# Optimization experiments

Measured on AMD Instinct MI355X. Metric: run time of the kernel, lower is better.

## Reference

```python
import jax, jax.numpy as jnp
import numpy as np


def _knn_ood(embeddings, bank, k, out_h, out_w):
    # embeddings: [B, D, h, w] ; bank: [N, D]
    B, D, h, w = embeddings.shape
    q = embeddings.transpose(0, 2, 3, 1).reshape(B * h * w, D)  # [Q, D] queries (per-pixel)
    # squared euclidean via ||q||^2 + ||b||^2 - 2 q.b (single GEMM, no python loop over batch)
    q2 = jnp.sum(q * q, axis=1, keepdims=True)                  # [Q, 1]
    b2 = jnp.sum(bank * bank, axis=1)[None, :]                  # [1, N]
    d2 = q2 + b2 - 2.0 * (q @ bank.T)                           # [Q, N]
    d = jnp.sqrt(jnp.maximum(d2, 1e-12))                        # euclidean, like sklearn
    neg_topk, _ = jax.lax.top_k(-d, k)                          # k smallest distances
    scores = jnp.mean(-neg_topk, axis=1).reshape(B, 1, h, w)    # mean distance to k-NN
    # F.interpolate(..., mode='bilinear', align_corners=False) == half-pixel bilinear resize
    return jax.image.resize(scores, (B, 1, out_h, out_w), method="bilinear")


def setup_inputs() -> dict:
    key = jax.random.key(0)
    k1, k2 = jax.random.split(key)
    B, D, h, w = 4, 128, 32, 32
    N = 50000
    return {
        "embeddings": jax.random.normal(k1, (B, D, h, w), dtype=jnp.float32),
        "bank": jax.random.normal(k2, (N, D), dtype=jnp.float32),
        "k": 5,
        "out_h": 512,
        "out_w": 512,
    }


def reference(embeddings, bank, k, out_h, out_w):
    return _knn_ood(embeddings, bank, k, out_h, out_w)
```

## Files before the change

### kernel.cpp

```cpp
#include <hip/hip_runtime.h>

typedef unsigned short u16;
typedef __attribute__((ext_vector_type(4))) unsigned short u16x4;
typedef __attribute__((ext_vector_type(8))) unsigned short u16x8;
typedef __attribute__((ext_vector_type(8))) __bf16 bf16x8;
typedef __attribute__((ext_vector_type(4))) float f32x4;

#define N_BANK  50000
#define NPAD    50048
#define NCHUNKS 782
#define SEGS    32
#define NCPAD   800
#define DIM     128
#define NQ      4096
#define CHUNK_B 16384

#define WS_BANKBF 0u
#define WS_B2     12812288u
#define WS_QBF    13012480u
#define WS_Q2     14061056u
#define WS_SCORES 14077440u
#define WS_MINBUF 14093824u
#define WS_NEED_PAIRS 27201024u

__device__ __forceinline__ u16 f2bf(float f) {
  unsigned int x = __float_as_uint(f);
  x += 0x7fffu + ((x >> 16) & 1u);
  return (u16)(x >> 16);
}
__device__ __forceinline__ u16 f2bf_up(float f) {
  unsigned int b = __float_as_uint(f);
  u16 h = (u16)(b >> 16);
  if (!(b >> 31) && (b & 0xffffu)) h++;
  return h;
}
__device__ __forceinline__ float bf2f(u16 h) {
  return __uint_as_float(((unsigned int)h) << 16);
}

#define SINS5(T0, T1, T2, T3, T4, x)                                  \
  {                                                                   \
    bool c3 = (x) < T3, c2 = (x) < T2, c1 = (x) < T1, c0 = (x) < T0;  \
    float nx_ = fminf((x), T4);                                       \
    T4 = c3 ? T3 : nx_;                                               \
    T3 = c3 ? (c2 ? T2 : (x)) : T3;                                   \
    T2 = c2 ? (c1 ? T1 : (x)) : T2;                                   \
    T1 = c1 ? (c0 ? T0 : (x)) : T1;                                   \
    T0 = c0 ? (x) : T0;                                               \
  }

__device__ __forceinline__ void gload_lds16(const void* g, void* l) {
  __builtin_amdgcn_global_load_lds(
      (const __attribute__((address_space(1))) void*)g,
      (__attribute__((address_space(3))) void*)l, 16, 0, 0);
}

__global__ __launch_bounds__(256) void prep_bank(const float* __restrict__ bank,
                                                 u16* __restrict__ bb,
                                                 float* __restrict__ b2) {
  int row = blockIdx.x * 8 + (threadIdx.x >> 5);
  int cc  = threadIdx.x & 31;
  bool valid = row < N_BANK;
  f32x4 v = f32x4{0.f, 0.f, 0.f, 0.f};
  if (valid) v = *reinterpret_cast<const f32x4*>(bank + (size_t)row * DIM + cc * 4);
  float s = v.x * v.x + v.y * v.y + v.z * v.z + v.w * v.w;
#pragma unroll
  for (int o = 16; o > 0; o >>= 1) s += __shfl_xor(s, o, 32);
  u16x4 u;
  u.x = f2bf(v.x); u.y = f2bf(v.y); u.z = f2bf(v.z); u.w = f2bf(v.w);
  *reinterpret_cast<u16x4*>(bb + (size_t)row * DIM + cc * 4) = u;
  if (cc == 0) b2[row] = valid ? s : 1e30f;
}

__global__ __launch_bounds__(256) void prep_q(const float* __restrict__ emb,
                                              u16* __restrict__ qb,
                                              float* __restrict__ q2) {
  int q = blockIdx.x * 256 + threadIdx.x;
  int b = q >> 10, yx = q & 1023;
  const float* src = emb + (size_t)b * 131072 + yx;
  float s = 0.f;
#pragma unroll
  for (int d0 = 0; d0 < 16; ++d0) {
    u16x8 u;
#pragma unroll
    for (int j = 0; j < 8; ++j) {
      float v = src[(d0 * 8 + j) * 1024];
      s += v * v;
      u[j] = f2bf(v);
    }
    *reinterpret_cast<u16x8*>(qb + (size_t)q * DIM + d0 * 8) = u;
  }
  q2[q] = s;
}

template <bool PAIRS>
__global__ __launch_bounds__(512) void pass1_kernel(const u16* __restrict__ bankbf,
                                                    const float* __restrict__ b2,
                                                    const u16* __restrict__ qbf,
                                                    void* __restrict__ minbuf) {
  __shared__ char smc[2 * CHUNK_B];
  __shared__ unsigned int mintile[6400];
  const int tid = threadIdx.x;
  const int w = tid >> 6, l = tid & 63;
  const int l15 = l & 15, lhi = l >> 4;
  const int qgi = blockIdx.x & 15, seg = blockIdx.x >> 4;
  const int qbase = qgi * 256 + w * 32;

  for (int i = tid; i < 6400; i += 512) mintile[i] = 0x7F807F80u;

  bf16x8 bqA[4], bqB[4];
  {
    const u16* qa = qbf + (size_t)(qbase + l15) * DIM + lhi * 8;
#pragma unroll
    for (int kk = 0; kk < 4; ++kk) {
      bqA[kk] = *reinterpret_cast<const bf16x8*>(qa + kk * 32);
      bqB[kk] = *reinterpret_cast<const bf16x8*>(qa + 16 * DIM + kk * 32);
    }
  }

  auto stage = [&](int cc, int buf) {
    const char* gb = (const char*)bankbf + (size_t)cc * CHUNK_B;
#pragma unroll
    for (int i = 0; i < 2; ++i) {
      int x  = i * 8192 + tid * 16;
      int sx = x ^ (((x >> 8) & 7) << 4);
      gload_lds16(gb + sx, smc + buf * CHUNK_B + i * 8192 + w * 1024);
    }
  };

  stage(seg, 0);
  __syncthreads();
  int cur = 0;
  int s = 0;
  for (int c = seg; c < NCHUNKS; c += SEGS, ++s) {
    if (c + SEGS < NCHUNKS) stage(c + SEGS, cur ^ 1);
    const char* sb = smc + cur * CHUNK_B;
    float m1A = 3e38f, m2A = 3e38f, m1B = 3e38f, m2B = 3e38f;
#pragma unroll
    for (int t = 0; t < 4; ++t) {
      f32x4 b2v = *reinterpret_cast<const f32x4*>(b2 + c * 64 + t * 16 + lhi * 4);
      bf16x8 af[4];
#pragma unroll
      for (int kk = 0; kk < 4; ++kk) {
        int p  = (t * 16 + l15) * 256 + kk * 64 + lhi * 16;
        int ph = p ^ (((p >> 8) & 7) << 4);
        af[kk] = *reinterpret_cast<const bf16x8*>(sb + ph);
      }
      f32x4 accA = f32x4{0.f, 0.f, 0.f, 0.f};
      f32x4 accB = f32x4{0.f, 0.f, 0.f, 0.f};
#pragma unroll
      for (int kk = 0; kk < 4; ++kk) {
        accA = __builtin_amdgcn_mfma_f32_16x16x32_bf16(af[kk], bqA[kk], accA, 0, 0, 0);
        accB = __builtin_amdgcn_mfma_f32_16x16x32_bf16(af[kk], bqB[kk], accB, 0, 0, 0);
      }
#pragma unroll
      for (int j = 0; j < 4; ++j) {
        float sA = fmaf(-2.f, accA[j], b2v[j]);
        float sB = fmaf(-2.f, accB[j], b2v[j]);
        if (PAIRS) {
          float t1 = fminf(m1A, sA);
          m2A = fminf(m2A, fmaxf(m1A, sA));
          m1A = t1;
          float t2 = fminf(m1B, sB);
          m2B = fminf(m2B, fmaxf(m1B, sB));
          m1B = t2;
        } else {
          m1A = fminf(m1A, sA);
          m1B = fminf(m1B, sB);
        }
      }
    }
#pragma unroll
    for (int o = 16; o <= 32; o <<= 1) {
      float o1 = __shfl_xor(m1A, o);
      if (PAIRS) {
        float o2 = __shfl_xor(m2A, o);
        m2A = fminf(fminf(m2A, o2), fmaxf(m1A, o1));
      }
      m1A = fminf(m1A, o1);
      float p1 = __shfl_xor(m1B, o);
      if (PAIRS) {
        float p2 = __shfl_xor(m2B, o);
        m2B = fminf(fminf(m2B, p2), fmaxf(m1B, p1));
      }
      m1B = fminf(m1B, p1);
    }
    if (l < 16) {
      unsigned int pA, pB;
      if (PAIRS) {
        pA = ((unsigned int)f2bf(m2A) << 16) | (unsigned int)f2bf(m1A);
        pB = ((unsigned int)f2bf(m2B) << 16) | (unsigned int)f2bf(m1B);
      } else {
        pA = f2bf_up(m1A);
        pB = f2bf_up(m1B);
      }
      mintile[(w * 32 + l) * 25 + s] = pA;
      mintile[(w * 32 + 16 + l) * 25 + s] = pB;
    }
    __syncthreads();
    cur ^= 1;
  }

  if (PAIRS) {
    unsigned int* mb = (unsigned int*)minbuf;
    for (int i = tid; i < 6400; i += 512) {
      int qloc = i / 25, j = i - qloc * 25;
      mb[(size_t)(qgi * 256 + qloc) * NCPAD + seg * 25 + j] = mintile[i];
    }
  } else {
    u16* mb = (u16*)minbuf;
    for (int i = tid; i < 6400; i += 512) {
      int qloc = i / 25, j = i - qloc * 25;
      mb[(size_t)(qgi * 256 + qloc) * NCPAD + seg * 25 + j] = (u16)mintile[i];
    }
  }
}

template <bool PAIRS>
__global__ __launch_bounds__(256) void pass2_kernel(const u16* __restrict__ bankbf,
                                                    const float* __restrict__ b2,
                                                    const u16* __restrict__ qbf,
                                                    const float* __restrict__ q2,
                                                    const void* __restrict__ minbuf,
                                                    float* __restrict__ scores) {
  const int w = threadIdx.x >> 6, l = threadIdx.x & 63;
  const int q = blockIdx.x * 4 + w;

  unsigned int vals[13];
  if (PAIRS) {
    const unsigned int* row = (const unsigned int*)minbuf + (size_t)q * NCPAD;
#pragma unroll
    for (int r = 0; r < 13; ++r) {
      int col = r * 64 + l;
      vals[r] = (col < NCPAD) ? row[col] : 0x7F807F80u;
    }
  } else {
    const u16* row = (const u16*)minbuf + (size_t)q * NCPAD;
#pragma unroll
    for (int r = 0; r < 13; ++r) {
      int col = r * 64 + l;
      vals[r] = (col < NCPAD) ? (unsigned int)row[col] : 0x7F80u;
    }
  }

  float T0 = 3e38f, T1 = 3e38f, T2_ = 3e38f, T3 = 3e38f, T4 = 3e38f;
#pragma unroll
  for (int r = 0; r < 13; ++r) {
    float m1v = bf2f((u16)(vals[r] & 0xffffu));
    SINS5(T0, T1, T2_, T3, T4, m1v);
    if (PAIRS) {
      float m2v = bf2f((u16)(vals[r] >> 16));
      SINS5(T0, T1, T2_, T3, T4, m2v);
    }
  }
#pragma unroll
  for (int sft = 1; sft < 64; sft <<= 1) {
    float p0 = __shfl_xor(T0, sft), p1 = __shfl_xor(T1, sft), p2 = __shfl_xor(T2_, sft),
          p3 = __shfl_xor(T3, sft), p4 = __shfl_xor(T4, sft);
    SINS5(T0, T1, T2_, T3, T4, p0);
    SINS5(T0, T1, T2_, T3, T4, p1);
    SINS5(T0, T1, T2_, T3, T4, p2);
    SINS5(T0, T1, T2_, T3, T4, p3);
    SINS5(T0, T1, T2_, T3, T4, p4);
  }
  const float thr = PAIRS ? (T4 + fabsf(T4) * 0.01f + 2.5f)
                          : (T4 + fabsf(T4) * 0.01f + 0.02f);

  float F0 = 3e38f, F1 = 3e38f, F2_ = 3e38f, F3 = 3e38f, F4 = 3e38f;
  unsigned long long msk[13];
  unsigned long long anym = 0ull;
#pragma unroll
  for (int r = 0; r < 13; ++r) {
    float m1v = bf2f((u16)(vals[r] & 0xffffu));
    bool flag;
    if (PAIRS) {
      float m2v = bf2f((u16)(vals[r] >> 16));
      flag = (m2v <= thr);
      if (!flag) {
        SINS5(F0, F1, F2_, F3, F4, m1v);
        SINS5(F0, F1, F2_, F3, F4, m2v);
      }
    } else {
      flag = (m1v <= thr);
    }
    msk[r] = __ballot(flag);
    anym |= msk[r];
  }

  if (anym) {
    u16x8 qu[16];
#pragma unroll
    for (int g = 0; g < 16; ++g)
      qu[g] = *reinterpret_cast<const u16x8*>(qbf + (size_t)q * DIM + g * 8);
    for (int r = 0; r < 13; ++r) {
      unsigned long long mset = msk[r];
      while (mset) {
        int bit = __ffsll((long long)mset) - 1;
        mset &= mset - 1;
        int col = r * 64 + bit;
        int sgi = col / 25, sj = col - sgi * 25;
        int chunk = sgi + sj * SEGS;
        int rowid = chunk * 64 + l;
        const u16x8* bp = (const u16x8*)(bankbf + (size_t)rowid * DIM);
        float dot = 0.f;
#pragma unroll
        for (int g = 0; g < 16; ++g) {
          u16x8 bb = bp[g];
#pragma unroll
          for (int e = 0; e < 8; ++e)
            dot = fmaf(bf2f(bb[e]), bf2f(qu[g][e]), dot);
        }
        float d = fmaf(-2.f, dot, b2[rowid]);
        SINS5(F0, F1, F2_, F3, F4, d);
      }
    }
  }
#pragma unroll
  for (int sft = 1; sft < 64; sft <<= 1) {
    float p0 = __shfl_xor(F0, sft), p1 = __shfl_xor(F1, sft), p2 = __shfl_xor(F2_, sft),
          p3 = __shfl_xor(F3, sft), p4 = __shfl_xor(F4, sft);
    SINS5(F0, F1, F2_, F3, F4, p0);
    SINS5(F0, F1, F2_, F3, F4, p1);
    SINS5(F0, F1, F2_, F3, F4, p2);
    SINS5(F0, F1, F2_, F3, F4, p3);
    SINS5(F0, F1, F2_, F3, F4, p4);
  }
  if (l == 0) {
    float q2v = q2[q];
    float sc = sqrtf(fmaxf(q2v + F0, 1e-12f)) + sqrtf(fmaxf(q2v + F1, 1e-12f)) +
               sqrtf(fmaxf(q2v + F2_, 1e-12f)) + sqrtf(fmaxf(q2v + F3, 1e-12f)) +
               sqrtf(fmaxf(q2v + F4, 1e-12f));
    scores[q] = sc * 0.2f;
  }
}

__global__ __launch_bounds__(256) void resize_kernel(const float* __restrict__ scores,
                                                     float* __restrict__ out) {
  int idx = blockIdx.x * 256 + threadIdx.x;
  int b = idx >> 18;
  int rem = idx & 262143;
  int oy = rem >> 9, ox = rem & 511;
  float sx = (ox + 0.5f) * 0.0625f - 0.5f;
  float sy = (oy + 0.5f) * 0.0625f - 0.5f;
  float fx0 = floorf(sx), fy0 = floorf(sy);
  int x0 = (int)fx0, y0 = (int)fy0;
  float fx = sx - fx0, fy = sy - fy0;
  int x0c = x0 < 0 ? 0 : (x0 > 31 ? 31 : x0);
  int x1c = (x0 + 1) < 0 ? 0 : ((x0 + 1) > 31 ? 31 : (x0 + 1));
  int y0c = y0 < 0 ? 0 : (y0 > 31 ? 31 : y0);
  int y1c = (y0 + 1) < 0 ? 0 : ((y0 + 1) > 31 ? 31 : (y0 + 1));
  const float* sb = scores + (b << 10);
  float v00 = sb[y0c * 32 + x0c], v01 = sb[y0c * 32 + x1c];
  float v10 = sb[y1c * 32 + x0c], v11 = sb[y1c * 32 + x1c];
  float v0 = v00 + (v01 - v00) * fx;
  float v1 = v10 + (v11 - v10) * fx;
  out[idx] = v0 + (v1 - v0) * fy;
}

extern "C" void kernel_launch(void* const* d_in, const int* in_sizes, int n_in,
                              void* d_out, int out_size, void* d_ws, size_t ws_size,
                              hipStream_t stream) {
  const float* emb  = (const float*)d_in[0];
  const float* bank = (const float*)d_in[1];
  float* out = (float*)d_out;
  char* ws = (char*)d_ws;

  u16*   bankbf = (u16*)(ws + WS_BANKBF);
  float* b2     = (float*)(ws + WS_B2);
  u16*   qbf    = (u16*)(ws + WS_QBF);
  float* q2     = (float*)(ws + WS_Q2);
  float* scores = (float*)(ws + WS_SCORES);
  void*  minbuf = (void*)(ws + WS_MINBUF);

  prep_bank<<<NPAD / 8, 256, 0, stream>>>(bank, bankbf, b2);
  prep_q<<<NQ / 256, 256, 0, stream>>>(emb, qbf, q2);
  if (ws_size >= (size_t)WS_NEED_PAIRS) {
    pass1_kernel<true><<<16 * SEGS, 512, 0, stream>>>(bankbf, b2, qbf, minbuf);
    pass2_kernel<true><<<NQ / 4, 256, 0, stream>>>(bankbf, b2, qbf, q2, minbuf, scores);
  } else {
    pass1_kernel<false><<<16 * SEGS, 512, 0, stream>>>(bankbf, b2, qbf, minbuf);
    pass2_kernel<false><<<NQ / 4, 256, 0, stream>>>(bankbf, b2, qbf, q2, minbuf, scores);
  }
  resize_kernel<<<(NQ * 256) / 256, 256, 0, stream>>>(scores, out);
}
```

Before: 177.0 us.

## Fuse prep kernels, widen pass1 query tiles, fold -2 scaling, vectorize resize

```diff
diff --git a/kernel.cpp b/kernel.cpp
--- a/kernel.cpp
+++ b/kernel.cpp
@@ -14,6 +14,8 @@
 #define DIM     128
 #define NQ      4096
 #define CHUNK_B 16384
+#define NBANKBLK 6256
+#define NQBLK    64
 
 #define WS_BANKBF 0u
 #define WS_B2     12812288u
@@ -21,18 +23,11 @@
 #define WS_Q2     14061056u
 #define WS_SCORES 14077440u
 #define WS_MINBUF 14093824u
-#define WS_NEED_PAIRS 27201024u
 
 __device__ __forceinline__ u16 f2bf(float f) {
   unsigned int x = __float_as_uint(f);
   x += 0x7fffu + ((x >> 16) & 1u);
   return (u16)(x >> 16);
-}
-__device__ __forceinline__ u16 f2bf_up(float f) {
-  unsigned int b = __float_as_uint(f);
-  u16 h = (u16)(b >> 16);
-  if (!(b >> 31) && (b & 0xffffu)) h++;
-  return h;
 }
 __device__ __forceinline__ float bf2f(u16 h) {
   return __uint_as_float(((unsigned int)h) << 16);
@@ -55,203 +50,196 @@
       (__attribute__((address_space(3))) void*)l, 16, 0, 0);
 }
 
-__global__ __launch_bounds__(256) void prep_bank(const float* __restrict__ bank,
-                                                 u16* __restrict__ bb,
-                                                 float* __restrict__ b2) {
-  int row = blockIdx.x * 8 + (threadIdx.x >> 5);
-  int cc  = threadIdx.x & 31;
-  bool valid = row < N_BANK;
-  f32x4 v = f32x4{0.f, 0.f, 0.f, 0.f};
-  if (valid) v = *reinterpret_cast<const f32x4*>(bank + (size_t)row * DIM + cc * 4);
-  float s = v.x * v.x + v.y * v.y + v.z * v.z + v.w * v.w;
-#pragma unroll
-  for (int o = 16; o > 0; o >>= 1) s += __shfl_xor(s, o, 32);
-  u16x4 u;
-  u.x = f2bf(v.x); u.y = f2bf(v.y); u.z = f2bf(v.z); u.w = f2bf(v.w);
-  *reinterpret_cast<u16x4*>(bb + (size_t)row * DIM + cc * 4) = u;
-  if (cc == 0) b2[row] = valid ? s : 1e30f;
-}
-
-__global__ __launch_bounds__(256) void prep_q(const float* __restrict__ emb,
-                                              u16* __restrict__ qb,
-                                              float* __restrict__ q2) {
-  int q = blockIdx.x * 256 + threadIdx.x;
-  int b = q >> 10, yx = q & 1023;
-  const float* src = emb + (size_t)b * 131072 + yx;
-  float s = 0.f;
-#pragma unroll
-  for (int d0 = 0; d0 < 16; ++d0) {
-    u16x8 u;
-#pragma unroll
-    for (int j = 0; j < 8; ++j) {
-      float v = src[(d0 * 8 + j) * 1024];
-      s += v * v;
-      u[j] = f2bf(v);
-    }
-    *reinterpret_cast<u16x8*>(qb + (size_t)q * DIM + d0 * 8) = u;
-  }
-  q2[q] = s;
-}
-
-template <bool PAIRS>
-__global__ __launch_bounds__(512) void pass1_kernel(const u16* __restrict__ bankbf,
-                                                    const float* __restrict__ b2,
-                                                    const u16* __restrict__ qbf,
-                                                    void* __restrict__ minbuf) {
+__global__ __launch_bounds__(256) void prep_kernel(const float* __restrict__ emb,
+                                                   const float* __restrict__ bank,
+                                                   u16* __restrict__ bb,
+                                                   float* __restrict__ b2,
+                                                   u16* __restrict__ qb,
+                                                   float* __restrict__ q2) {
+  const int tid = threadIdx.x;
+  if (blockIdx.x < NBANKBLK) {
+    int row = blockIdx.x * 8 + (tid >> 5);
+    int cc  = tid & 31;
+    bool valid = row < N_BANK;
+    f32x4 v = f32x4{0.f, 0.f, 0.f, 0.f};
+    if (valid) v = *reinterpret_cast<const f32x4*>(bank + (size_t)row * DIM + cc * 4);
+    float s = v.x * v.x + v.y * v.y + v.z * v.z + v.w * v.w;
+#pragma unroll
+    for (int o = 16; o > 0; o >>= 1) s += __shfl_xor(s, o, 32);
+    u16x4 u;
+    u.x = f2bf(-2.f * v.x); u.y = f2bf(-2.f * v.y);
+    u.z = f2bf(-2.f * v.z); u.w = f2bf(-2.f * v.w);
+    *reinterpret_cast<u16x4*>(bb + (size_t)row * DIM + cc * 4) = u;
+    if (cc == 0) b2[row] = valid ? s : 1e30f;
+  } else {
+    __shared__ float part[256];
+    int qb0 = (blockIdx.x - NBANKBLK) * 64;
+    int ql = tid & 63, p = tid >> 6;
+    int q = qb0 + ql;
+    int b = q >> 10, yx = q & 1023;
+    const float* src = emb + (size_t)b * 131072 + (size_t)p * 32 * 1024 + yx;
+    float s = 0.f;
+#pragma unroll
+    for (int d8 = 0; d8 < 4; ++d8) {
+      u16x8 u;
+#pragma unroll
+      for (int j = 0; j < 8; ++j) {
+        float v = src[(d8 * 8 + j) * 1024];
+        s += v * v;
+        u[j] = f2bf(v);
+      }
+      *reinterpret_cast<u16x8*>(qb + (size_t)q * DIM + p * 32 + d8 * 8) = u;
+    }
+    part[tid] = s;
+    __syncthreads();
+    if (p == 0) q2[q] = part[ql] + part[64 + ql] + part[128 + ql] + part[192 + ql];
+  }
+}
+
+__global__ __launch_bounds__(256, 2) void pass1_kernel(const u16* __restrict__ bankbf,
+                                                       const float* __restrict__ b2,
+                                                       const u16* __restrict__ qbf,
+                                                       unsigned int* __restrict__ minbuf) {
   __shared__ char smc[2 * CHUNK_B];
   __shared__ unsigned int mintile[6400];
   const int tid = threadIdx.x;
   const int w = tid >> 6, l = tid & 63;
   const int l15 = l & 15, lhi = l >> 4;
   const int qgi = blockIdx.x & 15, seg = blockIdx.x >> 4;
-  const int qbase = qgi * 256 + w * 32;
-
-  for (int i = tid; i < 6400; i += 512) mintile[i] = 0x7F807F80u;
-
-  bf16x8 bqA[4], bqB[4];
-  {
-    const u16* qa = qbf + (size_t)(qbase + l15) * DIM + lhi * 8;
+  const int qbase = qgi * 256 + w * 64;
+
+  for (int i = tid; i < 6400; i += 256) mintile[i] = 0x7F807F80u;
+
+  bf16x8 bq[16];
+#pragma unroll
+  for (int sg = 0; sg < 4; ++sg)
+#pragma unroll
+    for (int kk = 0; kk < 4; ++kk)
+      bq[sg * 4 + kk] = *reinterpret_cast<const bf16x8*>(
+          qbf + (size_t)(qbase + sg * 16 + l15) * DIM + kk * 32 + lhi * 8);
+
+  int ph[16];
+#pragma unroll
+  for (int t = 0; t < 4; ++t)
 #pragma unroll
     for (int kk = 0; kk < 4; ++kk) {
-      bqA[kk] = *reinterpret_cast<const bf16x8*>(qa + kk * 32);
-      bqB[kk] = *reinterpret_cast<const bf16x8*>(qa + 16 * DIM + kk * 32);
-    }
-  }
+      int p = (t * 16 + l15) * 256 + kk * 64 + lhi * 16;
+      ph[t * 4 + kk] = p ^ (((p >> 8) & 7) << 4);
+    }
 
   auto stage = [&](int cc, int buf) {
     const char* gb = (const char*)bankbf + (size_t)cc * CHUNK_B;
 #pragma unroll
-    for (int i = 0; i < 2; ++i) {
-      int x  = i * 8192 + tid * 16;
+    for (int i = 0; i < 4; ++i) {
+      int x  = i * 4096 + tid * 16;
       int sx = x ^ (((x >> 8) & 7) << 4);
-      gload_lds16(gb + sx, smc + buf * CHUNK_B + i * 8192 + w * 1024);
+      gload_lds16(gb + sx, smc + buf * CHUNK_B + i * 4096 + w * 1024);
     }
   };
-
+  auto loadb2 = [&](int cc, f32x4* dst) {
+#pragma unroll
+    for (int t = 0; t < 4; ++t)
+      dst[t] = *reinterpret_cast<const f32x4*>(b2 + cc * 64 + t * 16 + lhi * 4);
+  };
+
+  auto process = [&](const char* sb, const f32x4* bv, int s) {
+    float m1[4], m2[4];
+#pragma unroll
+    for (int sg = 0; sg < 4; ++sg) { m1[sg] = 3e38f; m2[sg] = 3e38f; }
+#pragma unroll
+    for (int t = 0; t < 4; ++t) {
+      bf16x8 af[4];
+#pragma unroll
+      for (int kk = 0; kk < 4; ++kk)
+        af[kk] = *reinterpret_cast<const bf16x8*>(sb + ph[t * 4 + kk]);
+      f32x4 acc[4];
+#pragma unroll
+      for (int sg = 0; sg < 4; ++sg) acc[sg] = bv[t];
+#pragma unroll
+      for (int kk = 0; kk < 4; ++kk)
+#pragma unroll
+        for (int sg = 0; sg < 4; ++sg)
+          acc[sg] = __builtin_amdgcn_mfma_f32_16x16x32_bf16(af[kk], bq[sg * 4 + kk],
+                                                            acc[sg], 0, 0, 0);
+#pragma unroll
+      for (int sg = 0; sg < 4; ++sg)
+#pragma unroll
+        for (int j = 0; j < 4; ++j) {
+          float sv = acc[sg][j];
+          float t1 = fminf(m1[sg], sv);
+          m2[sg] = fminf(m2[sg], fmaxf(m1[sg], sv));
+          m1[sg] = t1;
+        }
+    }
+#pragma unroll
+    for (int sg = 0; sg < 4; ++sg) {
+#pragma unroll
+      for (int o = 16; o <= 32; o <<= 1) {
+        float o1 = __shfl_xor(m1[sg], o);
+        float o2 = __shfl_xor(m2[sg], o);
+        m2[sg] = fminf(fminf(m2[sg], o2), fmaxf(m1[sg], o1));
+        m1[sg] = fminf(m1[sg], o1);
+      }
+      if (l < 16)
+        mintile[(w * 64 + sg * 16 + l15) * 25 + s] =
+            ((unsigned int)f2bf(m2[sg]) << 16) | (unsigned int)f2bf(m1[sg]);
+    }
+  };
+
+  f32x4 b2A[4], b2B[4];
   stage(seg, 0);
+  loadb2(seg, b2A);
   __syncthreads();
-  int cur = 0;
-  int s = 0;
-  for (int c = seg; c < NCHUNKS; c += SEGS, ++s) {
-    if (c + SEGS < NCHUNKS) stage(c + SEGS, cur ^ 1);
-    const char* sb = smc + cur * CHUNK_B;
-    float m1A = 3e38f, m2A = 3e38f, m1B = 3e38f, m2B = 3e38f;
-#pragma unroll
-    for (int t = 0; t < 4; ++t) {
-      f32x4 b2v = *reinterpret_cast<const f32x4*>(b2 + c * 64 + t * 16 + lhi * 4);
-      bf16x8 af[4];
-#pragma unroll
-      for (int kk = 0; kk < 4; ++kk) {
-        int p  = (t * 16 + l15) * 256 + kk * 64 + lhi * 16;
-        int ph = p ^ (((p >> 8) & 7) << 4);
-        af[kk] = *reinterpret_cast<const bf16x8*>(sb + ph);
-      }
-      f32x4 accA = f32x4{0.f, 0.f, 0.f, 0.f};
-      f32x4 accB = f32x4{0.f, 0.f, 0.f, 0.f};
-#pragma unroll
-      for (int kk = 0; kk < 4; ++kk) {
-        accA = __builtin_amdgcn_mfma_f32_16x16x32_bf16(af[kk], bqA[kk], accA, 0, 0, 0);
-        accB = __builtin_amdgcn_mfma_f32_16x16x32_bf16(af[kk], bqB[kk], accB, 0, 0, 0);
-      }
-#pragma unroll
-      for (int j = 0; j < 4; ++j) {
-        float sA = fmaf(-2.f, accA[j], b2v[j]);
-        float sB = fmaf(-2.f, accB[j], b2v[j]);
-        if (PAIRS) {
-          float t1 = fminf(m1A, sA);
-          m2A = fminf(m2A, fmaxf(m1A, sA));
-          m1A = t1;
-          float t2 = fminf(m1B, sB);
-          m2B = fminf(m2B, fmaxf(m1B, sB));
-          m1B = t2;
-        } else {
-          m1A = fminf(m1A, sA);
-          m1B = fminf(m1B, sB);
-        }
-      }
-    }
-#pragma unroll
-    for (int o = 16; o <= 32; o <<= 1) {
-      float o1 = __shfl_xor(m1A, o);
-      if (PAIRS) {
-        float o2 = __shfl_xor(m2A, o);
-        m2A = fminf(fminf(m2A, o2), fmaxf(m1A, o1));
-      }
-      m1A = fminf(m1A, o1);
-      float p1 = __shfl_xor(m1B, o);
-      if (PAIRS) {
-        float p2 = __shfl_xor(m2B, o);
-        m2B = fminf(fminf(m2B, p2), fmaxf(m1B, p1));
-      }
-      m1B = fminf(m1B, p1);
-    }
-    if (l < 16) {
-      unsigned int pA, pB;
-      if (PAIRS) {
-        pA = ((unsigned int)f2bf(m2A) << 16) | (unsigned int)f2bf(m1A);
-        pB = ((unsigned int)f2bf(m2B) << 16) | (unsigned int)f2bf(m1B);
-      } else {
-        pA = f2bf_up(m1A);
-        pB = f2bf_up(m1B);
-      }
-      mintile[(w * 32 + l) * 25 + s] = pA;
-      mintile[(w * 32 + 16 + l) * 25 + s] = pB;
-    }
+
+  int c = seg, s = 0;
+  for (;;) {
+    int c1 = c + SEGS;
+    bool h1 = c1 < NCHUNKS;
+    if (h1) { stage(c1, 1); loadb2(c1, b2B); }
+    process(smc, b2A, s);
     __syncthreads();
-    cur ^= 1;
-  }
-
-  if (PAIRS) {
-    unsigned int* mb = (unsigned int*)minbuf;
-    for (int i = tid; i < 6400; i += 512) {
-      int qloc = i / 25, j = i - qloc * 25;
-      mb[(size_t)(qgi * 256 + qloc) * NCPAD + seg * 25 + j] = mintile[i];
-    }
-  } else {
-    u16* mb = (u16*)minbuf;
-    for (int i = tid; i < 6400; i += 512) {
-      int qloc = i / 25, j = i - qloc * 25;
-      mb[(size_t)(qgi * 256 + qloc) * NCPAD + seg * 25 + j] = (u16)mintile[i];
-    }
-  }
-}
-
-template <bool PAIRS>
+    if (!h1) break;
+    int c2 = c1 + SEGS;
+    bool h2 = c2 < NCHUNKS;
+    if (h2) { stage(c2, 0); loadb2(c2, b2A); }
+    process(smc + CHUNK_B, b2B, s + 1);
+    __syncthreads();
+    if (!h2) break;
+    c = c2; s += 2;
+  }
+
+  for (int i = tid; i < 6400; i += 256) {
+    int qloc = i / 25, j = i - qloc * 25;
+    minbuf[(size_t)(qgi * 256 + qloc) * NCPAD + seg * 25 + j] = mintile[i];
+  }
+}
+
 __global__ __launch_bounds__(256) void pass2_kernel(const u16* __restrict__ bankbf,
                                                     const float* __restrict__ b2,
                                                     const u16* __restrict__ qbf,
                                                     const float* __restrict__ q2,
-                                                    const void* __restrict__ minbuf,
+                                                    const unsigned int* __restrict__ minbuf,
                                                     float* __restrict__ scores) {
   const int w = threadIdx.x >> 6, l = threadIdx.x & 63;
   const int q = blockIdx.x * 4 + w;
 
   unsigned int vals[13];
-  if (PAIRS) {
-    const unsigned int* row = (const unsigned int*)minbuf + (size_t)q * NCPAD;
+  {
+    const unsigned int* row = minbuf + (size_t)q * NCPAD;
 #pragma unroll
     for (int r = 0; r < 13; ++r) {
       int col = r * 64 + l;
       vals[r] = (col < NCPAD) ? row[col] : 0x7F807F80u;
     }
-  } else {
-    const u16* row = (const u16*)minbuf + (size_t)q * NCPAD;
-#pragma unroll
-    for (int r = 0; r < 13; ++r) {
-      int col = r * 64 + l;
-      vals[r] = (col < NCPAD) ? (unsigned int)row[col] : 0x7F80u;
-    }
   }
 
   float T0 = 3e38f, T1 = 3e38f, T2_ = 3e38f, T3 = 3e38f, T4 = 3e38f;
 #pragma unroll
   for (int r = 0; r < 13; ++r) {
     float m1v = bf2f((u16)(vals[r] & 0xffffu));
+    float m2v = bf2f((u16)(vals[r] >> 16));
     SINS5(T0, T1, T2_, T3, T4, m1v);
-    if (PAIRS) {
-      float m2v = bf2f((u16)(vals[r] >> 16));
-      SINS5(T0, T1, T2_, T3, T4, m2v);
-    }
+    SINS5(T0, T1, T2_, T3, T4, m2v);
   }
 #pragma unroll
   for (int sft = 1; sft < 64; sft <<= 1) {
@@ -263,8 +251,7 @@
     SINS5(T0, T1, T2_, T3, T4, p3);
     SINS5(T0, T1, T2_, T3, T4, p4);
   }
-  const float thr = PAIRS ? (T4 + fabsf(T4) * 0.01f + 2.5f)
-                          : (T4 + fabsf(T4) * 0.01f + 0.02f);
+  const float thr = T4 + fabsf(T4) * 0.01f + 2.5f;
 
   float F0 = 3e38f, F1 = 3e38f, F2_ = 3e38f, F3 = 3e38f, F4 = 3e38f;
   unsigned long long msk[13];
@@ -272,16 +259,11 @@
 #pragma unroll
   for (int r = 0; r < 13; ++r) {
     float m1v = bf2f((u16)(vals[r] & 0xffffu));
-    bool flag;
-    if (PAIRS) {
-      float m2v = bf2f((u16)(vals[r] >> 16));
-      flag = (m2v <= thr);
-      if (!flag) {
-        SINS5(F0, F1, F2_, F3, F4, m1v);
-        SINS5(F0, F1, F2_, F3, F4, m2v);
-      }
-    } else {
-      flag = (m1v <= thr);
+    float m2v = bf2f((u16)(vals[r] >> 16));
+    bool flag = (m2v <= thr);
+    if (!flag) {
+      SINS5(F0, F1, F2_, F3, F4, m1v);
+      SINS5(F0, F1, F2_, F3, F4, m2v);
     }
     msk[r] = __ballot(flag);
     anym |= msk[r];
@@ -302,7 +284,7 @@
         int chunk = sgi + sj * SEGS;
         int rowid = chunk * 64 + l;
         const u16x8* bp = (const u16x8*)(bankbf + (size_t)rowid * DIM);
-        float dot = 0.f;
+        float dot = b2[rowid];
 #pragma unroll
         for (int g = 0; g < 16; ++g) {
           u16x8 bb = bp[g];
@@ -310,8 +292,7 @@
           for (int e = 0; e < 8; ++e)
             dot = fmaf(bf2f(bb[e]), bf2f(qu[g][e]), dot);
         }
-        float d = fmaf(-2.f, dot, b2[rowid]);
-        SINS5(F0, F1, F2_, F3, F4, d);
+        SINS5(F0, F1, F2_, F3, F4, dot);
       }
     }
   }
@@ -337,24 +318,33 @@
 __global__ __launch_bounds__(256) void resize_kernel(const float* __restrict__ scores,
                                                      float* __restrict__ out) {
   int idx = blockIdx.x * 256 + threadIdx.x;
-  int b = idx >> 18;
-  int rem = idx & 262143;
-  int oy = rem >> 9, ox = rem & 511;
-  float sx = (ox + 0.5f) * 0.0625f - 0.5f;
+  int b = idx >> 16;
+  int rem = idx & 65535;
+  int oy = rem >> 7, qx = rem & 127;
   float sy = (oy + 0.5f) * 0.0625f - 0.5f;
-  float fx0 = floorf(sx), fy0 = floorf(sy);
-  int x0 = (int)fx0, y0 = (int)fy0;
-  float fx = sx - fx0, fy = sy - fy0;
-  int x0c = x0 < 0 ? 0 : (x0 > 31 ? 31 : x0);
-  int x1c = (x0 + 1) < 0 ? 0 : ((x0 + 1) > 31 ? 31 : (x0 + 1));
+  float fy0 = floorf(sy);
+  int y0 = (int)fy0;
+  float fy = sy - fy0;
   int y0c = y0 < 0 ? 0 : (y0 > 31 ? 31 : y0);
   int y1c = (y0 + 1) < 0 ? 0 : ((y0 + 1) > 31 ? 31 : (y0 + 1));
   const float* sb = scores + (b << 10);
-  float v00 = sb[y0c * 32 + x0c], v01 = sb[y0c * 32 + x1c];
-  float v10 = sb[y1c * 32 + x0c], v11 = sb[y1c * 32 + x1c];
-  float v0 = v00 + (v01 - v00) * fx;
-  float v1 = v10 + (v11 - v10) * fx;
-  out[idx] = v0 + (v1 - v0) * fy;
+  const float* r0 = sb + y0c * 32;
+  const float* r1 = sb + y1c * 32;
+  f32x4 o;
+#pragma unroll
+  for (int k = 0; k < 4; ++k) {
+    int ox = qx * 4 + k;
+    float sx = (ox + 0.5f) * 0.0625f - 0.5f;
+    float fx0 = floorf(sx);
+    int x0 = (int)fx0;
+    float fx = sx - fx0;
+    int x0c = x0 < 0 ? 0 : (x0 > 31 ? 31 : x0);
+    int x1c = (x0 + 1) < 0 ? 0 : ((x0 + 1) > 31 ? 31 : (x0 + 1));
+    float v0 = r0[x0c] + (r0[x1c] - r0[x0c]) * fx;
+    float v1 = r1[x0c] + (r1[x1c] - r1[x0c]) * fx;
+    o[k] = v0 + (v1 - v0) * fy;
+  }
+  *reinterpret_cast<f32x4*>(out + ((size_t)b << 18) + oy * 512 + qx * 4) = o;
 }
 
 extern "C" void kernel_launch(void* const* d_in, const int* in_sizes, int n_in,
@@ -370,16 +360,10 @@
   u16*   qbf    = (u16*)(ws + WS_QBF);
   float* q2     = (float*)(ws + WS_Q2);
   float* scores = (float*)(ws + WS_SCORES);
-  void*  minbuf = (void*)(ws + WS_MINBUF);
-
-  prep_bank<<<NPAD / 8, 256, 0, stream>>>(bank, bankbf, b2);
-  prep_q<<<NQ / 256, 256, 0, stream>>>(emb, qbf, q2);
-  if (ws_size >= (size_t)WS_NEED_PAIRS) {
-    pass1_kernel<true><<<16 * SEGS, 512, 0, stream>>>(bankbf, b2, qbf, minbuf);
-    pass2_kernel<true><<<NQ / 4, 256, 0, stream>>>(bankbf, b2, qbf, q2, minbuf, scores);
-  } else {
-    pass1_kernel<false><<<16 * SEGS, 512, 0, stream>>>(bankbf, b2, qbf, minbuf);
-    pass2_kernel<false><<<NQ / 4, 256, 0, stream>>>(bankbf, b2, qbf, q2, minbuf, scores);
-  }
-  resize_kernel<<<(NQ * 256) / 256, 256, 0, stream>>>(scores, out);
-}
+  unsigned int* minbuf = (unsigned int*)(ws + WS_MINBUF);
+
+  prep_kernel<<<NBANKBLK + NQBLK, 256, 0, stream>>>(emb, bank, bankbf, b2, qbf, q2);
+  pass1_kernel<<<16 * SEGS, 256, 0, stream>>>(bankbf, b2, qbf, minbuf);
+  pass2_kernel<<<NQ / 4, 256, 0, stream>>>(bankbf, b2, qbf, q2, minbuf, scores);
+  resize_kernel<<<(NQ * 256) / 1024, 256, 0, stream>>>(scores, out);
+}
```

Measured after the change: 170.5 us. 1.04x faster.
